# Kernel tuning notes

Measured on AMD Instinct MI355X. Metric: run time of the kernel, lower is better.

## Reference

```python
import jax, jax.numpy as jnp
import numpy as np
from itertools import combinations

DIM = 3
METRIC = np.array([1.0, 1.0, 1.0], dtype=np.float32)
KERNEL_SIZE = 7
C_IN, C_OUT = 32, 32
HIDDEN = 64
NUM_LAYERS = 4
N_GRID = KERNEL_SIZE ** DIM


def _build_cayley(dim, metric):
    blades = [()] + [c for r in range(1, dim + 1) for c in combinations(range(dim), r)]
    idx = {b: i for i, b in enumerate(blades)}
    n = len(blades)
    C = np.zeros((n, n, n), dtype=np.float32)
    for i, a in enumerate(blades):
        for j, b in enumerate(blades):
            arr = list(a) + list(b)
            sign = 1.0
            changed = True
            while changed:
                changed = False
                t = 0
                while t < len(arr) - 1:
                    if arr[t] == arr[t + 1]:
                        sign *= metric[arr[t]]
                        del arr[t:t + 2]
                        changed = True
                        break
                    if arr[t] > arr[t + 1]:
                        arr[t], arr[t + 1] = arr[t + 1], arr[t]
                        sign = -sign
                        changed = True
                    t += 1
            C[i, j, idx[tuple(arr)]] = sign
    grades = np.array([len(b) for b in blades])
    return C, grades

_C_LRO, GRADES = _build_cayley(DIM, METRIC)
CAYLEY = np.transpose(_C_LRO, (0, 2, 1))  # [left, out, right] (CEGNN convention)
N_BLADES = CAYLEY.shape[0]
N_GRADES = DIM + 1

# nonzero grade-triple paths of the Cayley tensor and blade-level path-id lookup
_gp = np.zeros((N_GRADES,) * 3, dtype=bool)
for a in range(N_GRADES):
    for b in range(N_GRADES):
        for c in range(N_GRADES):
            _gp[a, b, c] = np.any(CAYLEY[np.ix_(GRADES == a, GRADES == b, GRADES == c)] != 0)
PATHS = np.argwhere(_gp)
P = len(PATHS)
assert P == 20  # product_paths_sum for Cl(3,0)
_pid = -np.ones((N_GRADES,) * 3, dtype=np.int64)
for p, (a, b, c) in enumerate(PATHS):
    _pid[a, b, c] = p
BLADE_PID = _pid[GRADES[:, None, None], GRADES[None, :, None], GRADES[None, None, :]]
BLADE_PID = np.where(BLADE_PID < 0, P, BLADE_PID)  # P -> zero slot

# centered relative-position grid, (N, 1, dim)
_ax = np.arange(KERNEL_SIZE, dtype=np.float32) - (KERNEL_SIZE - 1) / 2.0
_grid = np.stack(np.meshgrid(*([_ax] * DIM), indexing='ij'), axis=-1).reshape(-1, DIM)
REL_POS = jnp.asarray(_grid[:, None, :])
CAYLEY_J = jnp.asarray(CAYLEY)
GRADE_ONEHOT = jnp.asarray((GRADES[:, None] == np.arange(N_GRADES)[None, :]).astype(np.float32))
FACTOR = 1.0 / np.sqrt(float(KERNEL_SIZE ** DIM))
BLADES_OF = {g: np.where(GRADES == g)[0] for g in range(N_GRADES)}


def embed_grade(x, g):
    out = jnp.zeros(x.shape[:-1] + (N_BLADES,), x.dtype)
    return out.at[..., BLADES_OF[g]].set(x)


def expand_paths(w):
    # (..., P) grade-path weights -> (..., B, B, B) blade-level weights
    wz = jnp.concatenate([w, jnp.zeros(w.shape[:-1] + (1,), w.dtype)], axis=-1)
    return wz[..., BLADE_PID]


def mv_linear(x, W, b):
    # grade-wise equivariant channel mixing; x: (N,Ci,B), W: (G,Co,Ci), bias on scalar blade
    y = jnp.einsum('boi,nib->nob', W[GRADES], x)
    return y.at[:, :, 0].add(b)


def mv_silu(x, a, b):
    # gate each grade by sigmoid of its (learned-scaled) squared norm
    qg = jnp.einsum('ncb,bg->ncg', x * x, GRADE_ONEHOT)
    gate = jax.nn.sigmoid(a * qg + b)
    return x * gate[:, :, GRADES]


def gp_layer(x, w):
    # fully-connected steerable geometric product; x: (N,C,B), w: (Co,C,P)
    wc = expand_paths(w) * CAYLEY_J  # (Co, C, B, B, B)
    y = jnp.einsum('nik,oikjm,nim->noj', x, wc, x)
    return y / np.sqrt(float(x.shape[1]))


def setup_inputs() -> dict:
    key = jax.random.key(0)
    ks = jax.random.split(key, 8)
    G, B, H, Pn = N_GRADES, N_BLADES, HIDDEN, P
    rn = lambda k, s, sc: jax.random.normal(k, s, dtype=jnp.float32) * sc
    ci1 = C_IN + 1
    return {
        'condition': rn(ks[0], (C_IN, B), 1.0),
        'rel_pos_sigma': jnp.ones((1, 1, 1), jnp.float32),
        'cayley_w': rn(ks[1], (C_OUT, C_IN, Pn), 1.0 / np.sqrt(C_IN)),
        'lin0_W': rn(ks[2], (G, H, ci1), 1.0 / np.sqrt(ci1)),
        'lin0_b': jnp.zeros((H,), jnp.float32),
        'act0_a': rn(ks[3], (H, G), 0.2),
        'act0_b': jnp.zeros((H, G), jnp.float32),
        'gps_w': rn(ks[4], (NUM_LAYERS, H, H, Pn), 0.5 / np.sqrt(H)),
        'lins_W': rn(ks[5], (NUM_LAYERS - 1, G, H, H), 1.0 / np.sqrt(H)),
        'lins_b': jnp.zeros((NUM_LAYERS - 1, H), jnp.float32),
        'acts_a': rn(ks[6], (NUM_LAYERS - 1, H, G), 0.2),
        'acts_b': jnp.zeros((NUM_LAYERS - 1, H, G), jnp.float32),
        'out_W': rn(ks[7], (G, C_OUT * C_IN, H), 1.0 / np.sqrt(H)),
        'out_b': jnp.zeros((C_OUT * C_IN,), jnp.float32),
        'shell_sigma': jnp.ones((1, C_OUT, C_IN, B), jnp.float32),
    }


def reference(condition, rel_pos_sigma, cayley_w, lin0_W, lin0_b, act0_a, act0_b,
              gps_w, lins_W, lins_b, acts_a, acts_b, out_W, out_b, shell_sigma):
    metric = jnp.asarray(METRIC)
    q = jnp.sum(metric * REL_POS * REL_POS, axis=-1, keepdims=True)  # (N,1,1)
    scalar = jnp.exp(-q / (2.0 * rel_pos_sigma ** 2))
    x = embed_grade(scalar, 0) + embed_grade(REL_POS, 1)  # (N,1,B)
    cond = jnp.broadcast_to(condition[None], (N_GRID,) + condition.shape)
    x = jnp.concatenate([x, cond], axis=1)  # (N, c_in+1, B)
    # kernel network: CEGNN blocks [MVLinear -> MVSiLU -> steerable geometric product]
    h = gp_layer(mv_silu(mv_linear(x, lin0_W, lin0_b), act0_a, act0_b), gps_w[0])
    for l in range(NUM_LAYERS - 1):
        h = gp_layer(mv_silu(mv_linear(h, lins_W[l], lins_b[l]), acts_a[l], acts_b[l]), gps_w[l + 1])
    k = mv_linear(h, out_W, out_b).reshape(N_GRID, C_OUT, C_IN, N_BLADES)
    # per-(c_out,c_in,blade) scalar radial shell
    shell = jnp.exp(-q.reshape(N_GRID, 1, 1, 1) / (shell_sigma ** 2))
    k = k * shell * FACTOR
    # kernel head: sparse weighted-Cayley contraction
    wc = expand_paths(cayley_w) * CAYLEY_J  # (c_out, c_in, B, B, B)
    K = jnp.einsum('noik,oiklm->olimn', k, wc)
    return K.reshape(C_OUT * N_BLADES, C_IN * N_BLADES, KERNEL_SIZE, KERNEL_SIZE, KERNEL_SIZE)
```

## Files before the change

### kernel.cpp

```cpp
#include <hip/hip_runtime.h>
#include <math.h>

#define NB 8
#define NGRID 343
#define HID 64
#define NPATH 20

struct Tab {
  int prod_idx[8][8];
  int prod_sgn[8][8];
  int pid[4][4][4];
  int grade[8];
  int kk_idx[8][8];
  int kk_sgn[8][8];
};

constexpr Tab make_tab() {
  Tab t{};
  int mask[8]  = {0,1,2,4,3,5,6,7};
  int idxof[8] = {0,1,2,4,3,5,6,7};
  for (int k = 0; k < 8; ++k) {
    int g = 0;
    for (int b = 0; b < 3; ++b) g += (mask[k] >> b) & 1;
    t.grade[k] = g;
  }
  for (int k = 0; k < 8; ++k)
    for (int m = 0; m < 8; ++m) {
      int A = mask[k], B = mask[m];
      t.prod_idx[k][m] = idxof[A ^ B];
      int c = 0;
      for (int i = 0; i < 3; ++i)
        if ((B >> i) & 1)
          for (int j = i + 1; j < 3; ++j)
            if ((A >> j) & 1) c++;
      t.prod_sgn[k][m] = (c & 1) ? -1 : 1;
    }
  int pc = 0;
  for (int a = 0; a < 4; ++a)
    for (int b = 0; b < 4; ++b)
      for (int c = 0; c < 4; ++c) {
        bool ok = false;
        for (int k = 0; k < 8; ++k)
          for (int m = 0; m < 8; ++m)
            if (t.grade[k] == a && t.grade[m] == c &&
                t.grade[t.prod_idx[k][m]] == b)
              ok = true;
        t.pid[a][b][c] = ok ? pc++ : NPATH;
      }
  for (int l = 0; l < 8; ++l)
    for (int m = 0; m < 8; ++m)
      for (int k = 0; k < 8; ++k)
        if (t.prod_idx[k][m] == l) {
          t.kk_idx[l][m] = k;
          t.kk_sgn[l][m] = t.prod_sgn[k][m];
        }
  return t;
}
constexpr Tab TB = make_tab();

#define OFF_LIN0T 0
#define OFF_LINST 8448
#define OFF_GPST  57600
#define OFF_OUTWT 385280
#define OFF_KWS   647424

__global__ void ccs_prep_kernel(const float* __restrict__ lin0_W,
                                const float* __restrict__ lins_W,
                                const float* __restrict__ gps_w,
                                const float* __restrict__ out_W,
                                float* __restrict__ ws) {
  const int TOT = 8448 + 49152 + 327680 + 262144;
  for (int d = blockIdx.x * blockDim.x + threadIdx.x; d < TOT;
       d += gridDim.x * blockDim.x) {
    float v;
    if (d < 8448) {
      int idx = d;
      int hh = idx & 63, ch = (idx >> 6) % 33, g = (idx >> 6) / 33;
      v = lin0_W[(g * 64 + hh) * 33 + ch];
    } else if (d < 8448 + 49152) {
      int idx = d - OFF_LINST;
      int hh = idx & 63, i = (idx >> 6) & 63, g = (idx >> 12) & 3, l = idx >> 14;
      v = lins_W[((l * 4 + g) * 64 + hh) * 64 + i];
    } else if (d < 8448 + 49152 + 327680) {
      int idx = d - OFF_GPST;
      int o = idx & 63, p = (idx >> 6) % 20, i = ((idx >> 6) / 20) & 63,
          l = idx / 81920;
      v = gps_w[((l * 64 + o) * 64 + i) * 20 + p];
    } else {
      int idx = d - OFF_OUTWT;
      int oc = idx & 1023, i = (idx >> 10) & 63, g = idx >> 16;
      v = out_W[(g * 1024 + oc) * 64 + i];
    }
    ws[d] = v;
  }
}

__launch_bounds__(256)
__global__ void ccs_net_kernel(const float* __restrict__ condition,
                               const float* __restrict__ rel_pos_sigma,
                               const float* __restrict__ lin0_b,
                               const float* __restrict__ act0_a,
                               const float* __restrict__ act0_b,
                               const float* __restrict__ lins_b,
                               const float* __restrict__ acts_a,
                               const float* __restrict__ acts_b,
                               const float* __restrict__ out_b,
                               const float* __restrict__ shell_sigma,
                               const float* __restrict__ ws,
                               float* __restrict__ kws) {
  const float* lin0t = ws + OFF_LIN0T;
  const float* linst = ws + OFF_LINST;
  const float* gpst  = ws + OFF_GPST;
  const float* outwt = ws + OFF_OUTWT;

  __shared__ float xb[33 * 8];
  __shared__ float F0[64 * 8];
  __shared__ float F1[64 * 8];
  __shared__ float part[4 * 64 * 8];

  const int n = blockIdx.x;
  const int tid = threadIdx.x;
  const int iz = n % 7, iy = (n / 7) % 7, ix = n / 49;
  const float px = (float)ix - 3.f, py = (float)iy - 3.f, pz = (float)iz - 3.f;
  const float q = px * px + py * py + pz * pz;
  const float sig = rel_pos_sigma[0];
  const float scal = expf(-q / (2.f * sig * sig));

  for (int t = tid; t < 264; t += 256) {
    int ch = t >> 3, b = t & 7;
    float v;
    if (ch == 0)
      v = (b == 0) ? scal : (b == 1) ? px : (b == 2) ? py : (b == 3) ? pz : 0.f;
    else
      v = condition[(ch - 1) * 8 + b];
    xb[t] = v;
  }
  __syncthreads();

  const int hh = tid & 63;
  const int brow = tid >> 6;

  #pragma unroll
  for (int rep = 0; rep < 2; ++rep) {
    int b = brow + 4 * rep;
    int g = TB.grade[b];
    float acc = (b == 0) ? lin0_b[hh] : 0.f;
    const float* wrow = lin0t + g * 33 * 64 + hh;
    #pragma unroll
    for (int ch = 0; ch < 33; ++ch)
      acc = fmaf(wrow[ch * 64], xb[ch * 8 + b], acc);
    F0[hh * 8 + b] = acc;
  }
  __syncthreads();

  auto silu = [&](const float* src, float* dst, const float* aa,
                  const float* bb) {
    #pragma unroll
    for (int rep = 0; rep < 2; ++rep) {
      int b = brow + 4 * rep;
      int g = TB.grade[b];
      int s0 = (g == 0) ? 0 : (g == 1) ? 1 : (g == 2) ? 4 : 7;
      int cnt = (g == 0 || g == 3) ? 1 : 3;
      float qg = 0.f;
      for (int u = 0; u < cnt; ++u) {
        float v = src[hh * 8 + s0 + u];
        qg = fmaf(v, v, qg);
      }
      float z = fmaf(aa[hh * 4 + g], qg, bb[hh * 4 + g]);
      float gate = 1.f / (1.f + expf(-z));
      dst[hh * 8 + b] = src[hh * 8 + b] * gate;
    }
  };

  auto lin = [&](const float* src, float* dst, const float* wt,
                 const float* bias) {
    #pragma unroll
    for (int rep = 0; rep < 2; ++rep) {
      int b = brow + 4 * rep;
      int g = TB.grade[b];
      float acc = (b == 0) ? bias[hh] : 0.f;
      const float* wrow = wt + g * 64 * 64 + hh;
      #pragma unroll
      for (int i = 0; i < 64; ++i)
        acc = fmaf(wrow[i * 64], src[i * 8 + b], acc);
      dst[hh * 8 + b] = acc;
    }
  };

  auto gp = [&](const float* src, float* dst, const float* wl) {
    const int o = tid & 63;
    const int isub = tid >> 6;
    float facc[8];
    #pragma unroll
    for (int j = 0; j < 8; ++j) facc[j] = 0.f;
    for (int it = 0; it < 16; ++it) {
      int i = isub * 16 + it;
      float x8[8];
      #pragma unroll
      for (int b = 0; b < 8; ++b) x8[b] = src[i * 8 + b];
      const float* wb = wl + i * 20 * 64 + o;
      float wp[20];
      #pragma unroll
      for (int p = 0; p < 20; ++p) wp[p] = wb[p * 64];
      #pragma unroll
      for (int k = 0; k < 8; ++k) {
        #pragma unroll
        for (int m = 0; m < 8; ++m) {
          const int j = TB.prod_idx[k][m];
          const int p = TB.pid[TB.grade[k]][TB.grade[j]][TB.grade[m]];
          float tp = x8[k] * x8[m];
          if (TB.prod_sgn[k][m] > 0)
            facc[j] = fmaf(tp, wp[p], facc[j]);
          else
            facc[j] = fmaf(-tp, wp[p], facc[j]);
        }
      }
    }
    #pragma unroll
    for (int j = 0; j < 8; ++j) part[(isub * 64 + o) * 8 + j] = facc[j];
    __syncthreads();
    #pragma unroll
    for (int rep = 0; rep < 2; ++rep) {
      int idx = tid + rep * 256;
      float s = part[idx] + part[idx + 512] + part[idx + 1024] +
                part[idx + 1536];
      dst[idx] = s * 0.125f;
    }
    __syncthreads();
  };

  silu(F0, F1, act0_a, act0_b);
  __syncthreads();
  gp(F1, F0, gpst + 0);

  float* f = F0;
  float* g_ = F1;
  for (int l = 0; l < 3; ++l) {
    lin(f, g_, linst + l * 16384, lins_b + l * 64);
    __syncthreads();
    silu(g_, f, acts_a + l * 256, acts_b + l * 256);
    __syncthreads();
    gp(f, g_, gpst + (l + 1) * 81920);
    float* t = f; f = g_; g_ = t;
  }

  const float FACTOR = 1.0f / sqrtf(343.0f);
  #pragma unroll
  for (int r = 0; r < 4; ++r) {
    int oc = tid + r * 256;
    float acc[8];
    #pragma unroll
    for (int b = 0; b < 8; ++b) acc[b] = 0.f;
    acc[0] = out_b[oc];
    #pragma unroll 8
    for (int i = 0; i < 64; ++i) {
      float w0 = outwt[(0 * 64 + i) * 1024 + oc];
      float w1 = outwt[(1 * 64 + i) * 1024 + oc];
      float w2 = outwt[(2 * 64 + i) * 1024 + oc];
      float w3 = outwt[(3 * 64 + i) * 1024 + oc];
      const float* h = f + i * 8;
      acc[0] = fmaf(w0, h[0], acc[0]);
      acc[1] = fmaf(w1, h[1], acc[1]);
      acc[2] = fmaf(w1, h[2], acc[2]);
      acc[3] = fmaf(w1, h[3], acc[3]);
      acc[4] = fmaf(w2, h[4], acc[4]);
      acc[5] = fmaf(w2, h[5], acc[5]);
      acc[6] = fmaf(w2, h[6], acc[6]);
      acc[7] = fmaf(w3, h[7], acc[7]);
    }
    float out8[8];
    #pragma unroll
    for (int b = 0; b < 8; ++b) {
      float ss = shell_sigma[oc * 8 + b];
      out8[b] = acc[b] * expf(-q / (ss * ss)) * FACTOR;
    }
    float4* dst = (float4*)(kws + ((size_t)oc * 343 + n) * 8);
    dst[0] = make_float4(out8[0], out8[1], out8[2], out8[3]);
    dst[1] = make_float4(out8[4], out8[5], out8[6], out8[7]);
  }
}

__launch_bounds__(64)
__global__ void ccs_expand_kernel(const float* __restrict__ cayley_w,
                                  const float* __restrict__ kws,
                                  float* __restrict__ out) {
  const int oi = blockIdx.x;
  const int o = oi >> 5, i = oi & 31;
  const int n = blockIdx.y * 64 + threadIdx.x;
  if (n >= NGRID) return;
  float cw[20];
  #pragma unroll
  for (int p = 0; p < 20; ++p) cw[p] = cayley_w[oi * 20 + p];
  const float* kp = kws + ((size_t)oi * 343 + n) * 8;
  float k8[8];
  #pragma unroll
  for (int b = 0; b < 8; ++b) k8[b] = kp[b];
  #pragma unroll
  for (int l = 0; l < 8; ++l) {
    #pragma unroll
    for (int m = 0; m < 8; ++m) {
      const int kk = TB.kk_idx[l][m];
      const int p = TB.pid[TB.grade[kk]][TB.grade[l]][TB.grade[m]];
      float v = k8[kk] * cw[p];
      if (TB.kk_sgn[l][m] < 0) v = -v;
      out[((size_t)((o * 8 + l) * 256 + i * 8 + m)) * 343 + n] = v;
    }
  }
}

extern "C" void kernel_launch(void* const* d_in, const int* in_sizes, int n_in,
                              void* d_out, int out_size, void* d_ws,
                              size_t ws_size, hipStream_t stream) {
  const float* condition     = (const float*)d_in[0];
  const float* rel_pos_sigma = (const float*)d_in[1];
  const float* cayley_w      = (const float*)d_in[2];
  const float* lin0_W        = (const float*)d_in[3];
  const float* lin0_b        = (const float*)d_in[4];
  const float* act0_a        = (const float*)d_in[5];
  const float* act0_b        = (const float*)d_in[6];
  const float* gps_w         = (const float*)d_in[7];
  const float* lins_W        = (const float*)d_in[8];
  const float* lins_b        = (const float*)d_in[9];
  const float* acts_a        = (const float*)d_in[10];
  const float* acts_b        = (const float*)d_in[11];
  const float* out_W         = (const float*)d_in[12];
  const float* out_b         = (const float*)d_in[13];
  const float* shell_sigma   = (const float*)d_in[14];

  float* ws = (float*)d_ws;
  float* kws = ws + OFF_KWS;
  float* out = (float*)d_out;

  ccs_prep_kernel<<<dim3(640), dim3(256), 0, stream>>>(lin0_W, lins_W, gps_w,
                                                       out_W, ws);
  ccs_net_kernel<<<dim3(343), dim3(256), 0, stream>>>(
      condition, rel_pos_sigma, lin0_b, act0_a, act0_b, lins_b, acts_a, acts_b,
      out_b, shell_sigma, ws, kws);
  ccs_expand_kernel<<<dim3(1024, 6), dim3(64), 0, stream>>>(cayley_w, kws, out);
}
```

Before: 217.1 us.

## Process two grid points per block to reuse weight loads across points

```diff
diff --git a/kernel.cpp b/kernel.cpp
--- a/kernel.cpp
+++ b/kernel.cpp
@@ -95,7 +95,7 @@
   }
 }
 
-__launch_bounds__(256)
+__launch_bounds__(512)
 __global__ void ccs_net_kernel(const float* __restrict__ condition,
                                const float* __restrict__ rel_pos_sigma,
                                const float* __restrict__ lin0_b,
@@ -114,90 +114,127 @@
   const float* outwt = ws + OFF_OUTWT;
 
   __shared__ float xb[33 * 8];
-  __shared__ float F0[64 * 8];
-  __shared__ float F1[64 * 8];
-  __shared__ float part[4 * 64 * 8];
-
-  const int n = blockIdx.x;
+  __shared__ float x0r[2][8];
+  __shared__ __align__(16) float F0[2 * 512];
+  __shared__ __align__(16) float F1[2 * 512];
+  __shared__ float part[2 * 8 * 8 * 64];
+
   const int tid = threadIdx.x;
-  const int iz = n % 7, iy = (n / 7) % 7, ix = n / 49;
-  const float px = (float)ix - 3.f, py = (float)iy - 3.f, pz = (float)iz - 3.f;
-  const float q = px * px + py * py + pz * pz;
+  const int n0 = blockIdx.x * 2;
+  const int n1 = n0 + 1;
+
   const float sig = rel_pos_sigma[0];
-  const float scal = expf(-q / (2.f * sig * sig));
-
-  for (int t = tid; t < 264; t += 256) {
+
+  float qq[2];
+  {
+    int iz = n0 % 7, iy = (n0 / 7) % 7, ix = n0 / 49;
+    float px = (float)ix - 3.f, py = (float)iy - 3.f, pz = (float)iz - 3.f;
+    qq[0] = px * px + py * py + pz * pz;
+  }
+  {
+    int nc = (n1 < NGRID) ? n1 : (NGRID - 1);
+    int iz = nc % 7, iy = (nc / 7) % 7, ix = nc / 49;
+    float px = (float)ix - 3.f, py = (float)iy - 3.f, pz = (float)iz - 3.f;
+    qq[1] = px * px + py * py + pz * pz;
+  }
+
+  for (int t = tid; t < 264; t += 512) {
     int ch = t >> 3, b = t & 7;
-    float v;
-    if (ch == 0)
-      v = (b == 0) ? scal : (b == 1) ? px : (b == 2) ? py : (b == 3) ? pz : 0.f;
-    else
-      v = condition[(ch - 1) * 8 + b];
-    xb[t] = v;
+    xb[t] = (ch == 0) ? 0.f : condition[(ch - 1) * 8 + b];
+  }
+  if (tid < 16) {
+    int pt = tid >> 3, b = tid & 7;
+    int nc = n0 + pt;
+    if (nc >= NGRID) nc = NGRID - 1;
+    int iz = nc % 7, iy = (nc / 7) % 7, ix = nc / 49;
+    float px = (float)ix - 3.f, py = (float)iy - 3.f, pz = (float)iz - 3.f;
+    float q = px * px + py * py + pz * pz;
+    float scal = expf(-q / (2.f * sig * sig));
+    x0r[pt][b] =
+        (b == 0) ? scal : (b == 1) ? px : (b == 2) ? py : (b == 3) ? pz : 0.f;
   }
   __syncthreads();
 
-  const int hh = tid & 63;
-  const int brow = tid >> 6;
-
-  #pragma unroll
-  for (int rep = 0; rep < 2; ++rep) {
-    int b = brow + 4 * rep;
-    int g = TB.grade[b];
-    float acc = (b == 0) ? lin0_b[hh] : 0.f;
-    const float* wrow = lin0t + g * 33 * 64 + hh;
-    #pragma unroll
-    for (int ch = 0; ch < 33; ++ch)
-      acc = fmaf(wrow[ch * 64], xb[ch * 8 + b], acc);
-    F0[hh * 8 + b] = acc;
+  const int b8 = tid & 7;
+  const int hh = (tid >> 3) & 63;
+  const int gb = TB.grade[b8];
+
+  {
+    const float* wrow = lin0t + gb * 33 * 64 + hh;
+    float w0 = wrow[0];
+    float a0 = w0 * x0r[0][b8];
+    float a1 = w0 * x0r[1][b8];
+    if (b8 == 0) {
+      float bb = lin0_b[hh];
+      a0 += bb;
+      a1 += bb;
+    }
+    #pragma unroll
+    for (int ch = 1; ch < 33; ++ch) {
+      float w = wrow[ch * 64];
+      float xv = xb[ch * 8 + b8];
+      a0 = fmaf(w, xv, a0);
+      a1 = fmaf(w, xv, a1);
+    }
+    F0[hh * 8 + b8] = a0;
+    F0[512 + hh * 8 + b8] = a1;
   }
   __syncthreads();
 
   auto silu = [&](const float* src, float* dst, const float* aa,
                   const float* bb) {
-    #pragma unroll
-    for (int rep = 0; rep < 2; ++rep) {
-      int b = brow + 4 * rep;
-      int g = TB.grade[b];
-      int s0 = (g == 0) ? 0 : (g == 1) ? 1 : (g == 2) ? 4 : 7;
-      int cnt = (g == 0 || g == 3) ? 1 : 3;
+    int s0 = (gb == 0) ? 0 : (gb == 1) ? 1 : (gb == 2) ? 4 : 7;
+    int cnt = (gb == 0 || gb == 3) ? 1 : 3;
+    float A = aa[hh * 4 + gb], B = bb[hh * 4 + gb];
+    #pragma unroll
+    for (int pt = 0; pt < 2; ++pt) {
       float qg = 0.f;
       for (int u = 0; u < cnt; ++u) {
-        float v = src[hh * 8 + s0 + u];
+        float v = src[pt * 512 + hh * 8 + s0 + u];
         qg = fmaf(v, v, qg);
       }
-      float z = fmaf(aa[hh * 4 + g], qg, bb[hh * 4 + g]);
+      float z = fmaf(A, qg, B);
       float gate = 1.f / (1.f + expf(-z));
-      dst[hh * 8 + b] = src[hh * 8 + b] * gate;
+      dst[pt * 512 + hh * 8 + b8] = src[pt * 512 + hh * 8 + b8] * gate;
     }
   };
 
   auto lin = [&](const float* src, float* dst, const float* wt,
                  const float* bias) {
-    #pragma unroll
-    for (int rep = 0; rep < 2; ++rep) {
-      int b = brow + 4 * rep;
-      int g = TB.grade[b];
-      float acc = (b == 0) ? bias[hh] : 0.f;
-      const float* wrow = wt + g * 64 * 64 + hh;
-      #pragma unroll
-      for (int i = 0; i < 64; ++i)
-        acc = fmaf(wrow[i * 64], src[i * 8 + b], acc);
-      dst[hh * 8 + b] = acc;
-    }
+    const float* wrow = wt + gb * 64 * 64 + hh;
+    float a0 = 0.f, a1 = 0.f;
+    if (b8 == 0) {
+      float bb = bias[hh];
+      a0 = bb;
+      a1 = bb;
+    }
+    #pragma unroll
+    for (int i = 0; i < 64; ++i) {
+      float w = wrow[i * 64];
+      a0 = fmaf(w, src[i * 8 + b8], a0);
+      a1 = fmaf(w, src[512 + i * 8 + b8], a1);
+    }
+    dst[hh * 8 + b8] = a0;
+    dst[512 + hh * 8 + b8] = a1;
   };
 
   auto gp = [&](const float* src, float* dst, const float* wl) {
     const int o = tid & 63;
     const int isub = tid >> 6;
-    float facc[8];
-    #pragma unroll
-    for (int j = 0; j < 8; ++j) facc[j] = 0.f;
-    for (int it = 0; it < 16; ++it) {
-      int i = isub * 16 + it;
-      float x8[8];
-      #pragma unroll
-      for (int b = 0; b < 8; ++b) x8[b] = src[i * 8 + b];
+    float fa[8], fb[8];
+    #pragma unroll
+    for (int j = 0; j < 8; ++j) {
+      fa[j] = 0.f;
+      fb[j] = 0.f;
+    }
+    for (int it = 0; it < 8; ++it) {
+      int i = isub * 8 + it;
+      float4 va0 = *(const float4*)(src + i * 8);
+      float4 va1 = *(const float4*)(src + i * 8 + 4);
+      float4 vb0 = *(const float4*)(src + 512 + i * 8);
+      float4 vb1 = *(const float4*)(src + 512 + i * 8 + 4);
+      float xA[8] = {va0.x, va0.y, va0.z, va0.w, va1.x, va1.y, va1.z, va1.w};
+      float xB[8] = {vb0.x, vb0.y, vb0.z, vb0.w, vb1.x, vb1.y, vb1.z, vb1.w};
       const float* wb = wl + i * 20 * 64 + o;
       float wp[20];
       #pragma unroll
@@ -208,23 +245,32 @@
         for (int m = 0; m < 8; ++m) {
           const int j = TB.prod_idx[k][m];
           const int p = TB.pid[TB.grade[k]][TB.grade[j]][TB.grade[m]];
-          float tp = x8[k] * x8[m];
-          if (TB.prod_sgn[k][m] > 0)
-            facc[j] = fmaf(tp, wp[p], facc[j]);
-          else
-            facc[j] = fmaf(-tp, wp[p], facc[j]);
+          if (TB.prod_sgn[k][m] > 0) {
+            fa[j] = fmaf(xA[k] * xA[m], wp[p], fa[j]);
+            fb[j] = fmaf(xB[k] * xB[m], wp[p], fb[j]);
+          } else {
+            fa[j] = fmaf(-xA[k] * xA[m], wp[p], fa[j]);
+            fb[j] = fmaf(-xB[k] * xB[m], wp[p], fb[j]);
+          }
         }
       }
     }
     #pragma unroll
-    for (int j = 0; j < 8; ++j) part[(isub * 64 + o) * 8 + j] = facc[j];
+    for (int j = 0; j < 8; ++j) {
+      part[isub * 512 + j * 64 + o] = fa[j];
+      part[4096 + isub * 512 + j * 64 + o] = fb[j];
+    }
     __syncthreads();
     #pragma unroll
-    for (int rep = 0; rep < 2; ++rep) {
-      int idx = tid + rep * 256;
-      float s = part[idx] + part[idx + 512] + part[idx + 1024] +
-                part[idx + 1536];
-      dst[idx] = s * 0.125f;
+    for (int r = 0; r < 2; ++r) {
+      int item = tid + r * 512;
+      int oo = item & 63;
+      int j = (item >> 6) & 7;
+      int pt = item >> 9;
+      const float* pp = part + pt * 4096 + j * 64 + oo;
+      float s = pp[0] + pp[512] + pp[1024] + pp[1536] + pp[2048] + pp[2560] +
+                pp[3072] + pp[3584];
+      dst[pt * 512 + oo * 8 + j] = s * 0.125f;
     }
     __syncthreads();
   };
@@ -246,37 +292,54 @@
 
   const float FACTOR = 1.0f / sqrtf(343.0f);
   #pragma unroll
-  for (int r = 0; r < 4; ++r) {
-    int oc = tid + r * 256;
-    float acc[8];
-    #pragma unroll
-    for (int b = 0; b < 8; ++b) acc[b] = 0.f;
-    acc[0] = out_b[oc];
-    #pragma unroll 8
+  for (int r = 0; r < 2; ++r) {
+    int oc = tid + r * 512;
+    float acc[2][8];
+    #pragma unroll
+    for (int pt = 0; pt < 2; ++pt)
+      #pragma unroll
+      for (int b = 0; b < 8; ++b) acc[pt][b] = 0.f;
+    {
+      float bb = out_b[oc];
+      acc[0][0] = bb;
+      acc[1][0] = bb;
+    }
+    #pragma unroll 4
     for (int i = 0; i < 64; ++i) {
       float w0 = outwt[(0 * 64 + i) * 1024 + oc];
       float w1 = outwt[(1 * 64 + i) * 1024 + oc];
       float w2 = outwt[(2 * 64 + i) * 1024 + oc];
       float w3 = outwt[(3 * 64 + i) * 1024 + oc];
-      const float* h = f + i * 8;
-      acc[0] = fmaf(w0, h[0], acc[0]);
-      acc[1] = fmaf(w1, h[1], acc[1]);
-      acc[2] = fmaf(w1, h[2], acc[2]);
-      acc[3] = fmaf(w1, h[3], acc[3]);
-      acc[4] = fmaf(w2, h[4], acc[4]);
-      acc[5] = fmaf(w2, h[5], acc[5]);
-      acc[6] = fmaf(w2, h[6], acc[6]);
-      acc[7] = fmaf(w3, h[7], acc[7]);
-    }
-    float out8[8];
-    #pragma unroll
-    for (int b = 0; b < 8; ++b) {
-      float ss = shell_sigma[oc * 8 + b];
-      out8[b] = acc[b] * expf(-q / (ss * ss)) * FACTOR;
-    }
-    float4* dst = (float4*)(kws + ((size_t)oc * 343 + n) * 8);
-    dst[0] = make_float4(out8[0], out8[1], out8[2], out8[3]);
-    dst[1] = make_float4(out8[4], out8[5], out8[6], out8[7]);
+      #pragma unroll
+      for (int pt = 0; pt < 2; ++pt) {
+        float4 h0 = *(const float4*)(f + pt * 512 + i * 8);
+        float4 h1 = *(const float4*)(f + pt * 512 + i * 8 + 4);
+        acc[pt][0] = fmaf(w0, h0.x, acc[pt][0]);
+        acc[pt][1] = fmaf(w1, h0.y, acc[pt][1]);
+        acc[pt][2] = fmaf(w1, h0.z, acc[pt][2]);
+        acc[pt][3] = fmaf(w1, h0.w, acc[pt][3]);
+        acc[pt][4] = fmaf(w2, h1.x, acc[pt][4]);
+        acc[pt][5] = fmaf(w2, h1.y, acc[pt][5]);
+        acc[pt][6] = fmaf(w2, h1.z, acc[pt][6]);
+        acc[pt][7] = fmaf(w3, h1.w, acc[pt][7]);
+      }
+    }
+    #pragma unroll
+    for (int pt = 0; pt < 2; ++pt) {
+      int n = n0 + pt;
+      if (n < NGRID) {
+        float q = qq[pt];
+        float out8[8];
+        #pragma unroll
+        for (int b = 0; b < 8; ++b) {
+          float ss = shell_sigma[oc * 8 + b];
+          out8[b] = acc[pt][b] * expf(-q / (ss * ss)) * FACTOR;
+        }
+        float4* dstp = (float4*)(kws + ((size_t)oc * 343 + n) * 8);
+        dstp[0] = make_float4(out8[0], out8[1], out8[2], out8[3]);
+        dstp[1] = make_float4(out8[4], out8[5], out8[6], out8[7]);
+      }
+    }
   }
 }
 
@@ -333,7 +396,7 @@
 
   ccs_prep_kernel<<<dim3(640), dim3(256), 0, stream>>>(lin0_W, lins_W, gps_w,
                                                        out_W, ws);
-  ccs_net_kernel<<<dim3(343), dim3(256), 0, stream>>>(
+  ccs_net_kernel<<<dim3((NGRID + 1) / 2), dim3(512), 0, stream>>>(
       condition, rel_pos_sigma, lin0_b, act0_a, act0_b, lins_b, acts_a, acts_b,
       out_b, shell_sigma, ws, kws);
   ccs_expand_kernel<<<dim3(1024, 6), dim3(64), 0, stream>>>(cayley_w, kws, out);
```

Result: slower. 229.8 us (+5.8%).
